# Kernel optimization log

Measured on AMD Instinct MI355X. Metric: run time of the kernel, lower is better.

The kernel has to match this reference:

```python
import jax, jax.numpy as jnp
import numpy as np

B, D = 2048, 1024
TEMP = 0.1
LAMBDA_CS_REG = 0.5


def setup_inputs() -> dict:
    key = jax.random.key(0)
    k1, k2, k3, k4, k5 = jax.random.split(key, 5)
    return {
        "english": jax.random.normal(k1, (B, D), dtype=jnp.float32),
        "etok": jax.random.normal(k2, (B, D), dtype=jnp.float32),
        "ktoe": jax.random.normal(k3, (B, D), dtype=jnp.float32),
        "korean": jax.random.normal(k4, (B, D), dtype=jnp.float32),
        "cs_ratios": jax.random.uniform(k5, (B,), dtype=jnp.float32),
    }


def _l2norm(x):
    return x / jnp.linalg.norm(x, axis=1, keepdims=True)


def reference(english, etok, ktoe, korean, cs_ratios):
    e = _l2norm(english)   # [B,D]
    et = _l2norm(etok)
    kt = _l2norm(ktoe)
    k = _l2norm(korean)
    bsz = e.shape[0]

    # Stack the 4 embedding types: order [english, korean, etok, ktoe]
    embs = jnp.stack([e, k, et, kt])           # [4,B,D]

    # Similarities of each anchor row i against every row j of every type t.
    S_e = jnp.einsum("bd,tnd->tbn", e, embs) / TEMP   # [4,B,B] english anchors
    S_k = jnp.einsum("bd,tnd->tbn", k, embs) / TEMP   # [4,B,B] korean anchors
    exp_Se = jnp.exp(S_e)
    exp_Sk = jnp.exp(S_k)

    diag_e = jnp.diagonal(exp_Se, axis1=1, axis2=2)   # [4,B] exp(sim(anchor_i, type_i))
    diag_k = jnp.diagonal(exp_Sk, axis1=1, axis2=2)

    # Negatives: all 4 types for every j != i.
    neg_e = exp_Se.sum(axis=(0, 2)) - diag_e.sum(axis=0)   # [B]
    neg_k = exp_Sk.sum(axis=(0, 2)) - diag_k.sum(axis=0)

    # Positives: eng anchor -> {etok_i, ktoe_i, korean_i}; kor anchor -> {etok_i, ktoe_i, english_i}
    num_e = diag_e[1] + diag_e[2] + diag_e[3]
    num_k = diag_k[0] + diag_k[2] + diag_k[3]

    loss_e = -jnp.log(num_e / (num_e + neg_e))
    loss_k = -jnp.log(num_k / (num_k + neg_k))
    contrastive_loss = (loss_e + loss_k).sum() / (2 * bsz)

    # Code-switch regularization
    r = cs_ratios[:, None]                              # [B,1]
    etok_reg = jnp.linalg.norm(et - (r * e + (1 - r) * k), axis=1)
    ktoe_reg = jnp.linalg.norm(kt - ((1 - r) * e + r * k), axis=1)
    cs_reg_loss = (etok_reg + ktoe_reg).sum() / bsz

    total_loss = contrastive_loss + LAMBDA_CS_REG * cs_reg_loss
    return total_loss, contrastive_loss, cs_reg_loss
```

## Files before the change

### kernel.cpp

```cpp
#include <hip/hip_runtime.h>
#include <hip/hip_bf16.h>
#include <math.h>

#define NB   2048
#define ND   1024
#define INV_TEMP 10.0f
#define LAMBDA_CS 0.5f

using short8  = __attribute__((ext_vector_type(8))) short;
using floatx4 = __attribute__((ext_vector_type(4))) float;

__device__ __forceinline__ ushort f32_to_bf16_rne(float f) {
  union { float f; unsigned u; } v; v.f = f;
  unsigned u = v.u;
  u += 0x7FFFu + ((u >> 16) & 1u);
  return (ushort)(u >> 16);
}

__global__ __launch_bounds__(256) void k_norm_reg(
    const float* __restrict__ e, const float* __restrict__ k,
    const float* __restrict__ et, const float* __restrict__ kt,
    const float* __restrict__ ratios,
    ushort* __restrict__ M, float* __restrict__ reg_partial)
{
  const int b = blockIdx.x, tid = threadIdx.x;
  const int wave = tid >> 6, lane = tid & 63;

  float4 ve  = ((const float4*)(e  + (size_t)b * ND))[tid];
  float4 vk  = ((const float4*)(k  + (size_t)b * ND))[tid];
  float4 vet = ((const float4*)(et + (size_t)b * ND))[tid];
  float4 vkt = ((const float4*)(kt + (size_t)b * ND))[tid];

  float s0 = ve.x*ve.x + ve.y*ve.y + ve.z*ve.z + ve.w*ve.w;
  float s1 = vk.x*vk.x + vk.y*vk.y + vk.z*vk.z + vk.w*vk.w;
  float s2 = vet.x*vet.x + vet.y*vet.y + vet.z*vet.z + vet.w*vet.w;
  float s3 = vkt.x*vkt.x + vkt.y*vkt.y + vkt.z*vkt.z + vkt.w*vkt.w;
  #pragma unroll
  for (int o = 1; o < 64; o <<= 1) {
    s0 += __shfl_xor(s0, o); s1 += __shfl_xor(s1, o);
    s2 += __shfl_xor(s2, o); s3 += __shfl_xor(s3, o);
  }
  __shared__ float red[4][4];
  if (lane == 0) { red[wave][0] = s0; red[wave][1] = s1; red[wave][2] = s2; red[wave][3] = s3; }
  __syncthreads();
  const float ie  = 1.0f / sqrtf(red[0][0] + red[1][0] + red[2][0] + red[3][0]);
  const float ik  = 1.0f / sqrtf(red[0][1] + red[1][1] + red[2][1] + red[3][1]);
  const float iet = 1.0f / sqrtf(red[0][2] + red[1][2] + red[2][2] + red[3][2]);
  const float ikt = 1.0f / sqrtf(red[0][3] + red[1][3] + red[2][3] + red[3][3]);

  {
    ushort o4[4];
    o4[0] = f32_to_bf16_rne(ve.x * ie);  o4[1] = f32_to_bf16_rne(ve.y * ie);
    o4[2] = f32_to_bf16_rne(ve.z * ie);  o4[3] = f32_to_bf16_rne(ve.w * ie);
    *(ushort4*)(M + ((size_t)0 * NB + b) * ND + tid * 4) = *(ushort4*)o4;
    o4[0] = f32_to_bf16_rne(vk.x * ik);  o4[1] = f32_to_bf16_rne(vk.y * ik);
    o4[2] = f32_to_bf16_rne(vk.z * ik);  o4[3] = f32_to_bf16_rne(vk.w * ik);
    *(ushort4*)(M + ((size_t)1 * NB + b) * ND + tid * 4) = *(ushort4*)o4;
    o4[0] = f32_to_bf16_rne(vet.x * iet); o4[1] = f32_to_bf16_rne(vet.y * iet);
    o4[2] = f32_to_bf16_rne(vet.z * iet); o4[3] = f32_to_bf16_rne(vet.w * iet);
    *(ushort4*)(M + ((size_t)2 * NB + b) * ND + tid * 4) = *(ushort4*)o4;
    o4[0] = f32_to_bf16_rne(vkt.x * ikt); o4[1] = f32_to_bf16_rne(vkt.y * ikt);
    o4[2] = f32_to_bf16_rne(vkt.z * ikt); o4[3] = f32_to_bf16_rne(vkt.w * ikt);
    *(ushort4*)(M + ((size_t)3 * NB + b) * ND + tid * 4) = *(ushort4*)o4;
  }

  const float r = ratios[b], rm = 1.0f - r;
  float a1 = 0.f, a2 = 0.f;
  {
    float en, kn, d1, d2;
    en = ve.x*ie; kn = vk.x*ik;
    d1 = vet.x*iet - (r*en + rm*kn); d2 = vkt.x*ikt - (rm*en + r*kn);
    a1 += d1*d1; a2 += d2*d2;
    en = ve.y*ie; kn = vk.y*ik;
    d1 = vet.y*iet - (r*en + rm*kn); d2 = vkt.y*ikt - (rm*en + r*kn);
    a1 += d1*d1; a2 += d2*d2;
    en = ve.z*ie; kn = vk.z*ik;
    d1 = vet.z*iet - (r*en + rm*kn); d2 = vkt.z*ikt - (rm*en + r*kn);
    a1 += d1*d1; a2 += d2*d2;
    en = ve.w*ie; kn = vk.w*ik;
    d1 = vet.w*iet - (r*en + rm*kn); d2 = vkt.w*ikt - (rm*en + r*kn);
    a1 += d1*d1; a2 += d2*d2;
  }
  #pragma unroll
  for (int o = 1; o < 64; o <<= 1) { a1 += __shfl_xor(a1, o); a2 += __shfl_xor(a2, o); }
  __shared__ float red2[4][2];
  if (lane == 0) { red2[wave][0] = a1; red2[wave][1] = a2; }
  __syncthreads();
  if (tid == 0) {
    float t1 = red2[0][0] + red2[1][0] + red2[2][0] + red2[3][0];
    float t2 = red2[0][1] + red2[1][1] + red2[2][1] + red2[3][1];
    reg_partial[b] = sqrtf(t1) + sqrtf(t2);
  }
}

__global__ __launch_bounds__(256) void k_gemm_exp_rowsum(
    const ushort* __restrict__ M,
    float* __restrict__ rsp,
    float* __restrict__ diag)
{
  __shared__ ushort As[128 * 32];
  __shared__ ushort Bs[128 * 32];
  __shared__ float redR[256];
  __shared__ float redC[256];

  int bx, by;
  {
    int idx = blockIdx.x;
    if (idx < 1024) { by = idx >> 5; bx = 32 + (idx & 31); }
    else {
      int t = idx - 1024; by = 0;
      while (t >= 32 - by) { t -= 32 - by; ++by; }
      bx = by + t;
    }
  }
  const bool sym = (bx < 32) && (bx > by);
  const int j0 = bx * 128;
  const int i0 = by * 128;

  const int tid  = threadIdx.x;
  const int wave = tid >> 6;
  const int lane = tid & 63;
  const int q = lane >> 4;
  const int m = lane & 15;
  const int wrow = (wave >> 1) * 64;
  const int wcol = (wave & 1) * 64;

  floatx4 acc[4][4] = {};

  const int srow = lane >> 2;
  const int scol = (lane & 3) ^ ((srow >> 1) & 3);
  const int c0 = wave * 2, c1 = c0 + 1;

  const ushort* gA = M + (size_t)i0 * ND;
  const ushort* gB = M + (size_t)j0 * ND;

  int aoff[4], boff[4];
  #pragma unroll
  for (int x = 0; x < 4; ++x) {
    const int sw = (q ^ ((m >> 1) & 3)) * 8;
    aoff[x] = (wrow + x * 16 + m) * 32 + sw;
    boff[x] = (wcol + x * 16 + m) * 32 + sw;
  }

  for (int k0 = 0; k0 < ND; k0 += 32) {
    __syncthreads();
    {
      const ushort* g = gA + (size_t)(c0 * 16 + srow) * ND + k0 + scol * 8;
      __builtin_amdgcn_global_load_lds(
          (const __attribute__((address_space(1))) unsigned int*)g,
          (__attribute__((address_space(3))) unsigned int*)&As[c0 * 512], 16, 0, 0);
    }
    {
      const ushort* g = gA + (size_t)(c1 * 16 + srow) * ND + k0 + scol * 8;
      __builtin_amdgcn_global_load_lds(
          (const __attribute__((address_space(1))) unsigned int*)g,
          (__attribute__((address_space(3))) unsigned int*)&As[c1 * 512], 16, 0, 0);
    }
    {
      const ushort* g = gB + (size_t)(c0 * 16 + srow) * ND + k0 + scol * 8;
      __builtin_amdgcn_global_load_lds(
          (const __attribute__((address_space(1))) unsigned int*)g,
          (__attribute__((address_space(3))) unsigned int*)&Bs[c0 * 512], 16, 0, 0);
    }
    {
      const ushort* g = gB + (size_t)(c1 * 16 + srow) * ND + k0 + scol * 8;
      __builtin_amdgcn_global_load_lds(
          (const __attribute__((address_space(1))) unsigned int*)g,
          (__attribute__((address_space(3))) unsigned int*)&Bs[c1 * 512], 16, 0, 0);
    }
    __syncthreads();

    short8 af[4], bf[4];
    #pragma unroll
    for (int x = 0; x < 4; ++x) {
      af[x] = *(const short8*)&As[aoff[x]];
      bf[x] = *(const short8*)&Bs[boff[x]];
    }
    #pragma unroll
    for (int mi = 0; mi < 4; ++mi)
      #pragma unroll
      for (int ni = 0; ni < 4; ++ni)
        acc[mi][ni] = __builtin_amdgcn_mfma_f32_16x16x32_bf16(
            af[mi], bf[ni], acc[mi][ni], 0, 0, 0);
  }

  float colAcc[4] = {0.f, 0.f, 0.f, 0.f};
  #pragma unroll
  for (int mi = 0; mi < 4; ++mi) {
    #pragma unroll
    for (int r = 0; r < 4; ++r) {
      const int ig = i0 + wrow + mi * 16 + q * 4 + r;
      float s = 0.f;
      #pragma unroll
      for (int ni = 0; ni < 4; ++ni) {
        float v = __expf(acc[mi][ni][r] * INV_TEMP);
        s += v;
        colAcc[ni] += v;
        const int jg = j0 + wcol + ni * 16 + m;
        if ((jg & (NB - 1)) == (ig & (NB - 1))) {
          diag[(((ig >> 11) << 2) + (jg >> 11)) * NB + (ig & (NB - 1))] = v;
        }
      }
      s += __shfl_xor(s, 1);
      s += __shfl_xor(s, 2);
      s += __shfl_xor(s, 4);
      s += __shfl_xor(s, 8);
      if (m == 0) redR[(wave & 1) * 128 + wrow + mi * 16 + q * 4 + r] = s;
    }
  }
  #pragma unroll
  for (int ni = 0; ni < 4; ++ni) {
    float c = colAcc[ni];
    c += __shfl_xor(c, 16);
    c += __shfl_xor(c, 32);
    if (q == 0) redC[(wave >> 1) * 128 + wcol + ni * 16 + m] = c;
  }
  __syncthreads();
  if (tid < 128) {
    rsp[(size_t)bx * 4096 + i0 + tid] = redR[tid] + redR[128 + tid];
    if (sym)
      rsp[(size_t)by * 4096 + j0 + tid] = redC[tid] + redC[128 + tid];
  }
}

__global__ __launch_bounds__(256) void k_rowloss(
    const float* __restrict__ rsp, const float* __restrict__ diag,
    float* __restrict__ loss_row)
{
  const int n = blockIdx.x * 256 + threadIdx.x;
  float se = 0.f, sk = 0.f;
  #pragma unroll 8
  for (int s = 0; s < 64; ++s) {
    se += rsp[s * 4096 + n];
    sk += rsp[s * 4096 + 2048 + n];
  }
  const float d_ee  = diag[0 * NB + n];
  const float d_ek  = diag[1 * NB + n];
  const float d_eet = diag[2 * NB + n];
  const float d_ekt = diag[3 * NB + n];
  const float d_kk  = diag[5 * NB + n];
  const float d_ket = diag[6 * NB + n];
  const float d_kkt = diag[7 * NB + n];
  const float num_e = d_ek + d_eet + d_ekt;
  const float den_e = se - d_ee;
  const float num_k = d_ek + d_ket + d_kkt;
  const float den_k = sk - d_kk;
  loss_row[n] = logf(den_e / num_e) + logf(den_k / num_k);
}

__global__ __launch_bounds__(256) void k_out(
    const float* __restrict__ loss_row, const float* __restrict__ reg_partial,
    float* __restrict__ out)
{
  const int tid = threadIdx.x;
  const int wave = tid >> 6, lane = tid & 63;
  float l = 0.f, g = 0.f;
  #pragma unroll
  for (int i = 0; i < 8; ++i) {
    l += loss_row[tid + i * 256];
    g += reg_partial[tid + i * 256];
  }
  #pragma unroll
  for (int o = 1; o < 64; o <<= 1) { l += __shfl_xor(l, o); g += __shfl_xor(g, o); }
  __shared__ float rl[4], rg[4];
  if (lane == 0) { rl[wave] = l; rg[wave] = g; }
  __syncthreads();
  if (tid == 0) {
    float contrastive = (rl[0] + rl[1] + rl[2] + rl[3]) * (1.0f / (2.0f * NB));
    float cs = (rg[0] + rg[1] + rg[2] + rg[3]) * (1.0f / NB);
    out[0] = contrastive + LAMBDA_CS * cs;
    out[1] = contrastive;
    out[2] = cs;
  }
}

extern "C" void kernel_launch(void* const* d_in, const int* in_sizes, int n_in,
                              void* d_out, int out_size, void* d_ws, size_t ws_size,
                              hipStream_t stream) {
  const float* english = (const float*)d_in[0];
  const float* etok    = (const float*)d_in[1];
  const float* ktoe    = (const float*)d_in[2];
  const float* korean  = (const float*)d_in[3];
  const float* ratios  = (const float*)d_in[4];

  char* ws = (char*)d_ws;
  const size_t OFF_M    = 0;
  const size_t OFF_RSP  = OFF_M + (size_t)8192 * 1024 * 2;
  const size_t OFF_DIAG = OFF_RSP + (size_t)64 * 4096 * 4;
  const size_t OFF_REG  = OFF_DIAG + 8 * NB * sizeof(float);
  const size_t OFF_LOSS = OFF_REG + NB * sizeof(float);

  ushort* M           = (ushort*)(ws + OFF_M);
  float* rsp          = (float*)(ws + OFF_RSP);
  float* diag         = (float*)(ws + OFF_DIAG);
  float* reg_partial  = (float*)(ws + OFF_REG);
  float* loss_row     = (float*)(ws + OFF_LOSS);

  k_norm_reg<<<dim3(NB), 256, 0, stream>>>(english, korean, etok, ktoe, ratios, M, reg_partial);
  k_gemm_exp_rowsum<<<dim3(1552), 256, 0, stream>>>(M, rsp, diag);
  k_rowloss<<<dim3(8), 256, 0, stream>>>(rsp, diag, loss_row);
  k_out<<<dim3(1), 256, 0, stream>>>(loss_row, reg_partial, (float*)d_out);
}
```

Before: 166.8 us.

## Switch similarity GEMM to FP8 MFMA and fuse row-loss and final reduction

Normalized embeddings are now stored as FP8 (e4m3) instead of bf16, and the GEMM uses the scaled 16x16x128 f8f6f4 MFMA with a 128-wide K tile, halving operand bytes and cutting K iterations. Per-tile row partials are accumulated with atomics into a single rowsum buffer. A last-block-done counter lets the final GEMM block compute the per-row losses and output, which removes two kernel launches. The trade-off is reduced precision in similarities that are scaled by 10 and exponentiated, plus the nondeterminism of float atomics.

```diff
diff --git a/kernel.cpp b/kernel.cpp
--- a/kernel.cpp
+++ b/kernel.cpp
@@ -6,25 +6,30 @@
 #define ND   1024
 #define INV_TEMP 10.0f
 #define LAMBDA_CS 0.5f
-
-using short8  = __attribute__((ext_vector_type(8))) short;
+#define GEMM_BLOCKS 1552
+
+using intx4   = __attribute__((ext_vector_type(4))) int;
+using intx8   = __attribute__((ext_vector_type(8))) int;
 using floatx4 = __attribute__((ext_vector_type(4))) float;
 
-__device__ __forceinline__ ushort f32_to_bf16_rne(float f) {
-  union { float f; unsigned u; } v; v.f = f;
-  unsigned u = v.u;
-  u += 0x7FFFu + ((u >> 16) & 1u);
-  return (ushort)(u >> 16);
-}
-
-__global__ __launch_bounds__(256) void k_norm_reg(
+__device__ __forceinline__ int pack4_fp8(float a, float b, float c, float d) {
+  int p = __builtin_amdgcn_cvt_pk_fp8_f32(a, b, 0, false);
+  p     = __builtin_amdgcn_cvt_pk_fp8_f32(c, d, p, true);
+  return p;
+}
+
+__global__ __launch_bounds__(256) void k_prep(
     const float* __restrict__ e, const float* __restrict__ k,
     const float* __restrict__ et, const float* __restrict__ kt,
     const float* __restrict__ ratios,
-    ushort* __restrict__ M, float* __restrict__ reg_partial)
+    unsigned char* __restrict__ M, float* __restrict__ reg_partial,
+    float* __restrict__ rowsum, unsigned* __restrict__ counter)
 {
   const int b = blockIdx.x, tid = threadIdx.x;
   const int wave = tid >> 6, lane = tid & 63;
+
+  if (b < 16) rowsum[b * 256 + tid] = 0.0f;
+  if (b == 16 && tid == 0) *counter = 0u;
 
   float4 ve  = ((const float4*)(e  + (size_t)b * ND))[tid];
   float4 vk  = ((const float4*)(k  + (size_t)b * ND))[tid];
@@ -48,21 +53,14 @@
   const float iet = 1.0f / sqrtf(red[0][2] + red[1][2] + red[2][2] + red[3][2]);
   const float ikt = 1.0f / sqrtf(red[0][3] + red[1][3] + red[2][3] + red[3][3]);
 
-  {
-    ushort o4[4];
-    o4[0] = f32_to_bf16_rne(ve.x * ie);  o4[1] = f32_to_bf16_rne(ve.y * ie);
-    o4[2] = f32_to_bf16_rne(ve.z * ie);  o4[3] = f32_to_bf16_rne(ve.w * ie);
-    *(ushort4*)(M + ((size_t)0 * NB + b) * ND + tid * 4) = *(ushort4*)o4;
-    o4[0] = f32_to_bf16_rne(vk.x * ik);  o4[1] = f32_to_bf16_rne(vk.y * ik);
-    o4[2] = f32_to_bf16_rne(vk.z * ik);  o4[3] = f32_to_bf16_rne(vk.w * ik);
-    *(ushort4*)(M + ((size_t)1 * NB + b) * ND + tid * 4) = *(ushort4*)o4;
-    o4[0] = f32_to_bf16_rne(vet.x * iet); o4[1] = f32_to_bf16_rne(vet.y * iet);
-    o4[2] = f32_to_bf16_rne(vet.z * iet); o4[3] = f32_to_bf16_rne(vet.w * iet);
-    *(ushort4*)(M + ((size_t)2 * NB + b) * ND + tid * 4) = *(ushort4*)o4;
-    o4[0] = f32_to_bf16_rne(vkt.x * ikt); o4[1] = f32_to_bf16_rne(vkt.y * ikt);
-    o4[2] = f32_to_bf16_rne(vkt.z * ikt); o4[3] = f32_to_bf16_rne(vkt.w * ikt);
-    *(ushort4*)(M + ((size_t)3 * NB + b) * ND + tid * 4) = *(ushort4*)o4;
-  }
+  *(int*)(M + ((size_t)0 * NB + b) * ND + tid * 4) =
+      pack4_fp8(ve.x * ie,  ve.y * ie,  ve.z * ie,  ve.w * ie);
+  *(int*)(M + ((size_t)1 * NB + b) * ND + tid * 4) =
+      pack4_fp8(vk.x * ik,  vk.y * ik,  vk.z * ik,  vk.w * ik);
+  *(int*)(M + ((size_t)2 * NB + b) * ND + tid * 4) =
+      pack4_fp8(vet.x * iet, vet.y * iet, vet.z * iet, vet.w * iet);
+  *(int*)(M + ((size_t)3 * NB + b) * ND + tid * 4) =
+      pack4_fp8(vkt.x * ikt, vkt.y * ikt, vkt.z * ikt, vkt.w * ikt);
 
   const float r = ratios[b], rm = 1.0f - r;
   float a1 = 0.f, a2 = 0.f;
@@ -93,15 +91,19 @@
   }
 }
 
-__global__ __launch_bounds__(256) void k_gemm_exp_rowsum(
-    const ushort* __restrict__ M,
-    float* __restrict__ rsp,
-    float* __restrict__ diag)
+__global__ __launch_bounds__(256) void k_gemm(
+    const unsigned char* __restrict__ M,
+    float* __restrict__ rowsum,
+    float* __restrict__ diag,
+    const float* __restrict__ reg_partial,
+    unsigned* __restrict__ counter,
+    float* __restrict__ out)
 {
-  __shared__ ushort As[128 * 32];
-  __shared__ ushort Bs[128 * 32];
+  __shared__ __align__(16) unsigned char As[128 * 128];
+  __shared__ __align__(16) unsigned char Bs[128 * 128];
   __shared__ float redR[256];
   __shared__ float redC[256];
+  __shared__ unsigned s_rank;
 
   int bx, by;
   {
@@ -127,61 +129,65 @@
 
   floatx4 acc[4][4] = {};
 
-  const int srow = lane >> 2;
-  const int scol = (lane & 3) ^ ((srow >> 1) & 3);
-  const int c0 = wave * 2, c1 = c0 + 1;
-
-  const ushort* gA = M + (size_t)i0 * ND;
-  const ushort* gB = M + (size_t)j0 * ND;
-
-  int aoff[4], boff[4];
+  int sOffA[4];
+  int ldsOff[4];
   #pragma unroll
   for (int x = 0; x < 4; ++x) {
-    const int sw = (q ^ ((m >> 1) & 3)) * 8;
-    aoff[x] = (wrow + x * 16 + m) * 32 + sw;
-    boff[x] = (wcol + x * 16 + m) * 32 + sw;
-  }
-
-  for (int k0 = 0; k0 < ND; k0 += 32) {
+    const int r = (wave * 4 + x) * 8 + (lane >> 3);
+    const int c = (lane & 7) ^ (r & 7);
+    sOffA[x]  = r * ND + c * 16;
+    ldsOff[x] = (wave * 4 + x) * 1024;
+  }
+
+  const unsigned char* gA = M + (size_t)i0 * ND;
+  const unsigned char* gB = M + (size_t)j0 * ND;
+
+  int aoff0[4], aoff1[4], boff0[4], boff1[4];
+  #pragma unroll
+  for (int x = 0; x < 4; ++x) {
+    const int ra = wrow + x * 16 + m;
+    aoff0[x] = ra * 128 + ((2 * q)     ^ (ra & 7)) * 16;
+    aoff1[x] = ra * 128 + ((2 * q + 1) ^ (ra & 7)) * 16;
+    const int rb = wcol + x * 16 + m;
+    boff0[x] = rb * 128 + ((2 * q)     ^ (rb & 7)) * 16;
+    boff1[x] = rb * 128 + ((2 * q + 1) ^ (rb & 7)) * 16;
+  }
+
+  for (int it = 0; it < 8; ++it) {
+    const int koff = it * 128;
     __syncthreads();
-    {
-      const ushort* g = gA + (size_t)(c0 * 16 + srow) * ND + k0 + scol * 8;
+    #pragma unroll
+    for (int x = 0; x < 4; ++x) {
       __builtin_amdgcn_global_load_lds(
-          (const __attribute__((address_space(1))) unsigned int*)g,
-          (__attribute__((address_space(3))) unsigned int*)&As[c0 * 512], 16, 0, 0);
-    }
-    {
-      const ushort* g = gA + (size_t)(c1 * 16 + srow) * ND + k0 + scol * 8;
+          (const __attribute__((address_space(1))) unsigned int*)(gA + sOffA[x] + koff),
+          (__attribute__((address_space(3))) unsigned int*)&As[ldsOff[x]], 16, 0, 0);
       __builtin_amdgcn_global_load_lds(
-          (const __attribute__((address_space(1))) unsigned int*)g,
-          (__attribute__((address_space(3))) unsigned int*)&As[c1 * 512], 16, 0, 0);
-    }
-    {
-      const ushort* g = gB + (size_t)(c0 * 16 + srow) * ND + k0 + scol * 8;
-      __builtin_amdgcn_global_load_lds(
-          (const __attribute__((address_space(1))) unsigned int*)g,
-          (__attribute__((address_space(3))) unsigned int*)&Bs[c0 * 512], 16, 0, 0);
-    }
-    {
-      const ushort* g = gB + (size_t)(c1 * 16 + srow) * ND + k0 + scol * 8;
-      __builtin_amdgcn_global_load_lds(
-          (const __attribute__((address_space(1))) unsigned int*)g,
-          (__attribute__((address_space(3))) unsigned int*)&Bs[c1 * 512], 16, 0, 0);
+          (const __attribute__((address_space(1))) unsigned int*)(gB + sOffA[x] + koff),
+          (__attribute__((address_space(3))) unsigned int*)&Bs[ldsOff[x]], 16, 0, 0);
     }
     __syncthreads();
 
-    short8 af[4], bf[4];
+    intx8 af[4], bf[4];
     #pragma unroll
     for (int x = 0; x < 4; ++x) {
-      af[x] = *(const short8*)&As[aoff[x]];
-      bf[x] = *(const short8*)&Bs[boff[x]];
+      intx4 lo = *(const intx4*)&As[aoff0[x]];
+      intx4 hi = *(const intx4*)&As[aoff1[x]];
+      af[x][0] = lo[0]; af[x][1] = lo[1]; af[x][2] = lo[2]; af[x][3] = lo[3];
+      af[x][4] = hi[0]; af[x][5] = hi[1]; af[x][6] = hi[2]; af[x][7] = hi[3];
+      lo = *(const intx4*)&Bs[boff0[x]];
+      hi = *(const intx4*)&Bs[boff1[x]];
+      bf[x][0] = lo[0]; bf[x][1] = lo[1]; bf[x][2] = lo[2]; bf[x][3] = lo[3];
+      bf[x][4] = hi[0]; bf[x][5] = hi[1]; bf[x][6] = hi[2]; bf[x][7] = hi[3];
     }
     #pragma unroll
     for (int mi = 0; mi < 4; ++mi)
       #pragma unroll
       for (int ni = 0; ni < 4; ++ni)
-        acc[mi][ni] = __builtin_amdgcn_mfma_f32_16x16x32_bf16(
-            af[mi], bf[ni], acc[mi][ni], 0, 0, 0);
+        acc[mi][ni] = __builtin_amdgcn_mfma_scale_f32_16x16x128_f8f6f4(
+            af[mi], bf[ni], acc[mi][ni],
+            0 , 0 ,
+            0, 0x7f7f7f7f,
+            0, 0x7f7f7f7f);
   }
 
   float colAcc[4] = {0.f, 0.f, 0.f, 0.f};
@@ -217,60 +223,50 @@
   }
   __syncthreads();
   if (tid < 128) {
-    rsp[(size_t)bx * 4096 + i0 + tid] = redR[tid] + redR[128 + tid];
+    atomicAdd(&rowsum[i0 + tid], redR[tid] + redR[128 + tid]);
     if (sym)
-      rsp[(size_t)by * 4096 + j0 + tid] = redC[tid] + redC[128 + tid];
-  }
-}
-
-__global__ __launch_bounds__(256) void k_rowloss(
-    const float* __restrict__ rsp, const float* __restrict__ diag,
-    float* __restrict__ loss_row)
-{
-  const int n = blockIdx.x * 256 + threadIdx.x;
-  float se = 0.f, sk = 0.f;
-  #pragma unroll 8
-  for (int s = 0; s < 64; ++s) {
-    se += rsp[s * 4096 + n];
-    sk += rsp[s * 4096 + 2048 + n];
-  }
-  const float d_ee  = diag[0 * NB + n];
-  const float d_ek  = diag[1 * NB + n];
-  const float d_eet = diag[2 * NB + n];
-  const float d_ekt = diag[3 * NB + n];
-  const float d_kk  = diag[5 * NB + n];
-  const float d_ket = diag[6 * NB + n];
-  const float d_kkt = diag[7 * NB + n];
-  const float num_e = d_ek + d_eet + d_ekt;
-  const float den_e = se - d_ee;
-  const float num_k = d_ek + d_ket + d_kkt;
-  const float den_k = sk - d_kk;
-  loss_row[n] = logf(den_e / num_e) + logf(den_k / num_k);
-}
-
-__global__ __launch_bounds__(256) void k_out(
-    const float* __restrict__ loss_row, const float* __restrict__ reg_partial,
-    float* __restrict__ out)
-{
-  const int tid = threadIdx.x;
-  const int wave = tid >> 6, lane = tid & 63;
-  float l = 0.f, g = 0.f;
-  #pragma unroll
-  for (int i = 0; i < 8; ++i) {
-    l += loss_row[tid + i * 256];
-    g += reg_partial[tid + i * 256];
-  }
-  #pragma unroll
-  for (int o = 1; o < 64; o <<= 1) { l += __shfl_xor(l, o); g += __shfl_xor(g, o); }
-  __shared__ float rl[4], rg[4];
-  if (lane == 0) { rl[wave] = l; rg[wave] = g; }
+      atomicAdd(&rowsum[j0 + tid], redC[tid] + redC[128 + tid]);
+  }
+
   __syncthreads();
   if (tid == 0) {
-    float contrastive = (rl[0] + rl[1] + rl[2] + rl[3]) * (1.0f / (2.0f * NB));
-    float cs = (rg[0] + rg[1] + rg[2] + rg[3]) * (1.0f / NB);
-    out[0] = contrastive + LAMBDA_CS * cs;
-    out[1] = contrastive;
-    out[2] = cs;
+    __threadfence();
+    s_rank = __hip_atomic_fetch_add(counter, 1u, __ATOMIC_ACQ_REL,
+                                    __HIP_MEMORY_SCOPE_AGENT);
+  }
+  __syncthreads();
+  if (s_rank == GEMM_BLOCKS - 1) {
+    float l = 0.f, g = 0.f;
+    #pragma unroll
+    for (int i = 0; i < 8; ++i) {
+      const int n = tid + i * 256;
+      float se = __hip_atomic_load(&rowsum[n],        __ATOMIC_RELAXED, __HIP_MEMORY_SCOPE_AGENT);
+      float sk = __hip_atomic_load(&rowsum[2048 + n], __ATOMIC_RELAXED, __HIP_MEMORY_SCOPE_AGENT);
+      float d_ee  = __hip_atomic_load(&diag[0 * NB + n], __ATOMIC_RELAXED, __HIP_MEMORY_SCOPE_AGENT);
+      float d_ek  = __hip_atomic_load(&diag[1 * NB + n], __ATOMIC_RELAXED, __HIP_MEMORY_SCOPE_AGENT);
+      float d_eet = __hip_atomic_load(&diag[2 * NB + n], __ATOMIC_RELAXED, __HIP_MEMORY_SCOPE_AGENT);
+      float d_ekt = __hip_atomic_load(&diag[3 * NB + n], __ATOMIC_RELAXED, __HIP_MEMORY_SCOPE_AGENT);
+      float d_kk  = __hip_atomic_load(&diag[5 * NB + n], __ATOMIC_RELAXED, __HIP_MEMORY_SCOPE_AGENT);
+      float d_ket = __hip_atomic_load(&diag[6 * NB + n], __ATOMIC_RELAXED, __HIP_MEMORY_SCOPE_AGENT);
+      float d_kkt = __hip_atomic_load(&diag[7 * NB + n], __ATOMIC_RELAXED, __HIP_MEMORY_SCOPE_AGENT);
+      float num_e = d_ek + d_eet + d_ekt;
+      float den_e = se - d_ee;
+      float num_k = d_ek + d_ket + d_kkt;
+      float den_k = sk - d_kk;
+      l += logf(den_e / num_e) + logf(den_k / num_k);
+      g += reg_partial[n];
+    }
+    #pragma unroll
+    for (int o = 1; o < 64; o <<= 1) { l += __shfl_xor(l, o); g += __shfl_xor(g, o); }
+    if ((tid & 63) == 0) { redR[tid >> 6] = l; redC[tid >> 6] = g; }
+    __syncthreads();
+    if (tid == 0) {
+      float contrastive = (redR[0] + redR[1] + redR[2] + redR[3]) * (1.0f / (2.0f * NB));
+      float cs = (redC[0] + redC[1] + redC[2] + redC[3]) * (1.0f / NB);
+      out[0] = contrastive + LAMBDA_CS * cs;
+      out[1] = contrastive;
+      out[2] = cs;
+    }
   }
 }
 
@@ -285,19 +281,19 @@
 
   char* ws = (char*)d_ws;
   const size_t OFF_M    = 0;
-  const size_t OFF_RSP  = OFF_M + (size_t)8192 * 1024 * 2;
-  const size_t OFF_DIAG = OFF_RSP + (size_t)64 * 4096 * 4;
+  const size_t OFF_RS   = OFF_M + (size_t)8192 * 1024;
+  const size_t OFF_DIAG = OFF_RS + 4096 * sizeof(float);
   const size_t OFF_REG  = OFF_DIAG + 8 * NB * sizeof(float);
-  const size_t OFF_LOSS = OFF_REG + NB * sizeof(float);
-
-  ushort* M           = (ushort*)(ws + OFF_M);
-  float* rsp          = (float*)(ws + OFF_RSP);
+  const size_t OFF_CNT  = OFF_REG + NB * sizeof(float);
+
+  unsigned char* M    = (unsigned char*)(ws + OFF_M);
+  float* rowsum       = (float*)(ws + OFF_RS);
   float* diag         = (float*)(ws + OFF_DIAG);
   float* reg_partial  = (float*)(ws + OFF_REG);
-  float* loss_row     = (float*)(ws + OFF_LOSS);
-
-  k_norm_reg<<<dim3(NB), 256, 0, stream>>>(english, korean, etok, ktoe, ratios, M, reg_partial);
-  k_gemm_exp_rowsum<<<dim3(1552), 256, 0, stream>>>(M, rsp, diag);
-  k_rowloss<<<dim3(8), 256, 0, stream>>>(rsp, diag, loss_row);
-  k_out<<<dim3(1), 256, 0, stream>>>(loss_row, reg_partial, (float*)d_out);
-}
+  unsigned* counter   = (unsigned*)(ws + OFF_CNT);
+
+  k_prep<<<dim3(NB), 256, 0, stream>>>(english, korean, etok, ktoe, ratios,
+                                       M, reg_partial, rowsum, counter);
+  k_gemm<<<dim3(GEMM_BLOCKS), 256, 0, stream>>>(M, rowsum, diag, reg_partial,
+                                                counter, (float*)d_out);
+}
```

Measured after the change: 208.4 us. 24.9% more time.
